# Optimization experiments

Measured on AMD Instinct MI355X. Metric: run time of the kernel, lower is better.

The kernel has to match this reference:

```python
import jax, jax.numpy as jnp
import numpy as np

N = 64        # SSM state size
L = 262144    # l_max / sequence length


def setup_inputs() -> dict:
    key = jax.random.key(0)
    ks = jax.random.split(key, 8)
    u = jax.random.normal(ks[0], (L,), dtype=jnp.float32)
    # HiPPO-DPLR style eigenvalue init
    Lambda_re = -0.5 * jnp.ones((N,), jnp.float32)
    Lambda_im = jnp.pi * jnp.arange(N, dtype=jnp.float32)
    P_re = jax.random.normal(ks[1], (N,), jnp.float32)
    P_im = jax.random.normal(ks[2], (N,), jnp.float32)
    B_re = jax.random.normal(ks[3], (N,), jnp.float32)
    B_im = jax.random.normal(ks[4], (N,), jnp.float32)
    C_ri = (0.5 ** 0.5) * jax.random.normal(ks[5], (N, 2), jnp.float32)  # C = C_ri[:,0] + i*C_ri[:,1]
    D = jnp.ones((1,), jnp.float32)
    log_step = jax.random.uniform(ks[6], (1,), jnp.float32,
                                  minval=float(np.log(0.001)), maxval=float(np.log(0.1)))
    return {"u": u, "Lambda_re": Lambda_re, "Lambda_im": Lambda_im,
            "P_re": P_re, "P_im": P_im, "B_re": B_re, "B_im": B_im,
            "C_ri": C_ri, "D": D, "log_step": log_step}


def _kernel_DPLR(Lambda, P, Q, B, C, step, l):
    # Evaluate the SSM generating function at the l roots of unity (bilinear discretization)
    Omega = jnp.exp((-2j * jnp.pi) * (jnp.arange(l) / l))          # (L,)
    g = (2.0 / step) * ((1.0 - Omega) / (1.0 + Omega))             # (L,)
    c = 2.0 / (1.0 + Omega)                                        # (L,)
    # Core Cauchy matrix: the single large (L, N) complex intermediate
    recip = 1.0 / (g[:, None] - Lambda[None, :])                   # (L, N)
    # Four Cauchy dot products fused into one thin matmul
    v = jnp.stack([C.conj() * B, C.conj() * P,
                   Q.conj() * B, Q.conj() * P], axis=1)            # (N, 4)
    k = recip @ v                                                  # (L, 4)
    k00, k01, k10, k11 = k[:, 0], k[:, 1], k[:, 2], k[:, 3]
    atRoots = c * (k00 - k01 * (1.0 / (1.0 + k11)) * k10)          # (L,)
    return jnp.fft.ifft(atRoots, l).real                           # (L,) real kernel


def _causal_convolution(u, K):
    l = u.shape[0]
    ud = jnp.fft.rfft(jnp.pad(u, (0, K.shape[0])))
    Kd = jnp.fft.rfft(jnp.pad(K, (0, l)))
    return jnp.fft.irfft(ud * Kd)[:l]


def reference(u, Lambda_re, Lambda_im, P_re, P_im, B_re, B_im, C_ri, D, log_step):
    Lambda = Lambda_re + 1j * Lambda_im
    P = P_re + 1j * P_im
    B = B_re + 1j * B_im
    C = C_ri[:, 0] + 1j * C_ri[:, 1]
    step = jnp.exp(log_step)                                       # (1,)
    K = _kernel_DPLR(Lambda, P, P, B, C, step, u.shape[0])
    return _causal_convolution(u, K) + D * u
```

## Files before the change

### kernel.cpp

```cpp
#include <hip/hip_runtime.h>
#include <math.h>

#define L_LEN  262144
#define NST    64
#define TPB    256
#define PI2F   6.2831853071795864769f
#define PIF    3.1415926535897932385f

__device__ inline float2 cmul(float2 a, float2 b) {
    return make_float2(a.x*b.x - a.y*b.y, a.x*b.y + a.y*b.x);
}

template<int M, int NF>
__device__ float2* lds_fft_r4(float2* b0, float2* b1, float sgn) {
    float2* src = b0; float2* dst = b1;
    int Ns = 1;
    while (Ns * 4 <= M) {
        __syncthreads();
        const int NB = NF * (M / 4);
        for (int bi = threadIdx.x; bi < NB; bi += TPB) {
            int f = bi / (M / 4);
            int j = bi & (M / 4 - 1);
            int r = j & (Ns - 1);
            const float2* s = src + f * M;
            float2 x0 = s[j];
            float2 x1 = s[j +     (M/4)];
            float2 x2 = s[j + 2 * (M/4)];
            float2 x3 = s[j + 3 * (M/4)];
            float ang = sgn * PI2F * ((float)r / (float)(4 * Ns));
            float sn, cs; __sincosf(ang, &sn, &cs);
            float2 w1 = make_float2(cs, sn);
            float2 w2 = cmul(w1, w1);
            float2 w3 = cmul(w2, w1);
            x1 = cmul(x1, w1); x2 = cmul(x2, w2); x3 = cmul(x3, w3);
            float2 t0 = make_float2(x0.x + x2.x, x0.y + x2.y);
            float2 t1 = make_float2(x0.x - x2.x, x0.y - x2.y);
            float2 t2 = make_float2(x1.x + x3.x, x1.y + x3.y);
            float2 t3 = make_float2(x1.x - x3.x, x1.y - x3.y);
            float2* d = dst + f * M + ((j - r) << 2) + r;
            d[0]      = make_float2(t0.x + t2.x, t0.y + t2.y);
            d[Ns]     = make_float2(t1.x - sgn * t3.y, t1.y + sgn * t3.x);
            d[2 * Ns] = make_float2(t0.x - t2.x, t0.y - t2.y);
            d[3 * Ns] = make_float2(t1.x + sgn * t3.y, t1.y - sgn * t3.x);
        }
        float2* t = src; src = dst; dst = t;
        Ns <<= 2;
    }
    if (Ns < M) {
        __syncthreads();
        const int NB = NF * (M / 2);
        for (int bi = threadIdx.x; bi < NB; bi += TPB) {
            int f = bi / (M / 2);
            int j = bi & (M / 2 - 1);
            const float2* s = src + f * M;
            float2 a = s[j];
            float2 b = s[j + M / 2];
            float ang = sgn * PI2F * ((float)j / (float)M);
            float sn, cs; __sincosf(ang, &sn, &cs);
            float2 wb = make_float2(cs * b.x - sn * b.y, cs * b.y + sn * b.x);
            float2* d = dst + f * M + j;
            d[0]     = make_float2(a.x + wb.x, a.y + wb.y);
            d[M / 2] = make_float2(a.x - wb.x, a.y - wb.y);
        }
        float2* t = src; src = dst; dst = t;
    }
    __syncthreads();
    return src;
}


__global__ __launch_bounds__(TPB) void k1_atroots(
    const float* __restrict__ Lre, const float* __restrict__ Lim,
    const float* __restrict__ Pre, const float* __restrict__ Pim,
    const float* __restrict__ Bre, const float* __restrict__ Bim,
    const float* __restrict__ Cri, const float* __restrict__ lstp,
    float2* __restrict__ Acm)
{
    __shared__ float4 cA[NST], cB[NST], cC[NST], cD[NST];
    const int t = threadIdx.x, bx = blockIdx.x;
    if (t < NST) {
        float lr = Lre[t], li = Lim[t];
        float pr = Pre[t], pi = Pim[t];
        float br = Bre[t], bi = Bim[t];
        float cr = Cri[2*t], ci = Cri[2*t+1];
        float dx = -lr;
        float v00x = cr*br + ci*bi, v00y = cr*bi - ci*br;
        float v01x = cr*pr + ci*pi, v01y = cr*pi - ci*pr;
        float v10x = pr*br + pi*bi, v10y = pr*bi - pi*br;
        float v11x = pr*pr + pi*pi;
        cA[t] = make_float4(li, dx*dx, dx*v11x, -v11x);
        cB[t] = make_float4(dx*v00x, v00y, dx*v00y, -v00x);
        cC[t] = make_float4(dx*v01x, v01y, dx*v01y, -v01x);
        cD[t] = make_float4(dx*v10x, v10y, dx*v10y, -v10x);
    }
    __syncthreads();
    const int c = bx >> 1;
    const int e = ((bx & 1) << 8) + t;
    const int j = c + (e << 9);
    const float invL = 1.0f / (float)L_LEN;
    float G2 = 2.0f / expf(lstp[0]);
    float h = PIF * ((float)j * invL);
    float sn, cs; __sincosf(h, &sn, &cs);
    float tn = sn * __frcp_rn(cs);
    tn = fminf(fmaxf(tn, -1e7f), 1e7f);
    float gi = G2 * tn;
    float k00x=0.f,k00y=0.f,k01x=0.f,k01y=0.f,k10x=0.f,k10y=0.f,k11x=0.f,k11y=0.f;
    #pragma unroll 4
    for (int n = 0; n < NST; ++n) {
        float4 a = cA[n];
        float dy   = gi - a.x;
        float iv   = __frcp_rn(fmaf(dy, dy, a.y));
        float ivdy = iv * dy;
        k11x = fmaf(iv, a.z, k11x);  k11y = fmaf(ivdy, a.w, k11y);
        float4 b = cB[n];
        k00x = fmaf(iv, b.x, fmaf(ivdy, b.y, k00x));
        k00y = fmaf(iv, b.z, fmaf(ivdy, b.w, k00y));
        float4 cc = cC[n];
        k01x = fmaf(iv, cc.x, fmaf(ivdy, cc.y, k01x));
        k01y = fmaf(iv, cc.z, fmaf(ivdy, cc.w, k01y));
        float4 d = cD[n];
        k10x = fmaf(iv, d.x, fmaf(ivdy, d.y, k10x));
        k10y = fmaf(iv, d.z, fmaf(ivdy, d.w, k10y));
    }
    float ax = 1.f + k11x, ay = k11y;
    float im = 1.f / (ax*ax + ay*ay);
    float tx = k01x*k10x - k01y*k10y;
    float ty = k01x*k10y + k01y*k10x;
    float wx = k00x - (tx*ax + ty*ay) * im;
    float wy = k00y - (ty*ax - tx*ay) * im;
    Acm[(c << 9) + e] = make_float2(wx - tn*wy, wy + tn*wx);
}

__global__ __launch_bounds__(TPB) void k2_pass1(
    const float* __restrict__ u, const float2* __restrict__ Acm,
    float2* __restrict__ T_K, float2* __restrict__ T_U, float2* __restrict__ T_Uo)
{
    __shared__ float2 b0[2048], b1[2048];
    const int t = threadIdx.x, bx = blockIdx.x;
    const int c0 = (bx & 255) << 1;
    const float invL = 1.0f / (float)L_LEN;
    if (bx < 256) {
        for (int i = t; i < 1024; i += TPB)
            b0[i] = Acm[((c0 + (i >> 9)) << 9) + (i & 511)];
        float2* r = lds_fft_r4<512, 2>(b0, b1, +1.f);
        for (int i = t; i < 1024; i += TPB) {
            int f = i & 1, k = i >> 1;
            int c = c0 + f;
            float ang = PI2F * ((float)(c * k) * invL);
            float sn, cs; __sincosf(ang, &sn, &cs);
            T_K[(k << 9) + c] = cmul(make_float2(cs, sn), r[(f << 9) + k]);
        }
    } else {
        for (int i = t; i < 1024; i += TPB) {
            int f = i & 1, e = i >> 1;
            int n = (c0 + f) + (e << 9);
            float uv = u[n];
            float sn, cs; __sincosf(PIF * ((float)n * invL), &sn, &cs);
            b0[(f << 9) + e]        = make_float2(uv, 0.f);
            b0[((2 + f) << 9) + e]  = make_float2(uv * cs, -uv * sn);
        }
        float2* r = lds_fft_r4<512, 4>(b0, b1, -1.f);
        for (int i = t; i < 2048; i += TPB) {
            int f = i & 1, k = (i >> 1) & 511, v = i >> 10;
            int c = c0 + f;
            float ang = -PI2F * ((float)(c * k) * invL);
            float sn, cs; __sincosf(ang, &sn, &cs);
            float2 val = cmul(make_float2(cs, sn), r[(((v << 1) + f) << 9) + k]);
            if (v == 0) T_U [(k << 9) + c] = val;
            else        T_Uo[(k << 9) + c] = val;
        }
    }
}

__global__ __launch_bounds__(TPB) void k3_mid(
    const float2* __restrict__ T_K, const float2* __restrict__ T_U,
    const float2* __restrict__ T_Uo,
    float2* __restrict__ T_Ko, float2* __restrict__ Ue, float2* __restrict__ Uo)
{
    __shared__ float2 b0[2048], b1[2048];
    const int t = threadIdx.x, bx = blockIdx.x;
    const int c0 = (bx & 255) << 1;
    const float invL = 1.0f / (float)L_LEN;
    if (bx < 256) {
        for (int i = t; i < 1024; i += TPB)
            b0[i] = T_K[((c0 + (i >> 9)) << 9) + (i & 511)];
        float2* r = lds_fft_r4<512, 2>(b0, b1, +1.f);
        float2* o = (r == b0) ? b1 : b0;
        for (int i = t; i < 1024; i += TPB) {
            int f = i >> 9, o1 = i & 511;
            int n = (c0 + f) + (o1 << 9);
            float K = r[i].x * invL;
            float sn, cs; __sincosf(PIF * ((float)n * invL), &sn, &cs);
            o[i] = make_float2(K * cs, -K * sn);
        }
        float2* r2 = lds_fft_r4<512, 2>(o, r, -1.f);
        for (int i = t; i < 1024; i += TPB) {
            int f = i & 1, k = i >> 1;
            int c = c0 + f;
            float ang = -PI2F * ((float)(c * k) * invL);
            float sn, cs; __sincosf(ang, &sn, &cs);
            T_Ko[(k << 9) + c] = cmul(make_float2(cs, sn), r2[(f << 9) + k]);
        }
    } else {
        for (int i = t; i < 2048; i += TPB) {
            int v = i >> 10, f = (i >> 9) & 1, e = i & 511;
            const float2* Tin = v ? T_Uo : T_U;
            b0[i] = Tin[((c0 + f) << 9) + e];
        }
        float2* r = lds_fft_r4<512, 4>(b0, b1, -1.f);
        for (int i = t; i < 2048; i += TPB) {
            int v = i >> 10, f = (i >> 9) & 1, k2 = i & 511;
            float2* Xo = v ? Uo : Ue;
            Xo[((c0 + f) << 9) + k2] = r[i];
        }
    }
}

__global__ __launch_bounds__(TPB) void k4_point_inv1(
    const float2* __restrict__ T_Ko, const float2* __restrict__ Ue,
    const float2* __restrict__ Uo, const float2* __restrict__ Acm,
    float2* __restrict__ T_Ve, float2* __restrict__ T_Vo)
{
    __shared__ float2 b0[2048], b1[2048];
    const int t = threadIdx.x, bx = blockIdx.x;
    const int kk0 = bx << 1;
    const float invL = 1.0f / (float)L_LEN;
    for (int i = t; i < 1024; i += TPB)
        b0[i] = T_Ko[((kk0 + (i >> 9)) << 9) + (i & 511)];
    float2* r = lds_fft_r4<512, 2>(b0, b1, -1.f);
    float2* o = (r == b0) ? b1 : b0;
    for (int i = t; i < 1024; i += TPB) {
        int f = i >> 9, k2 = i & 511;
        int kc = kk0 + f;
        float2 ko = r[i];
        float2 ue = Ue [(kc << 9) + k2];
        float2 uo = Uo [(kc << 9) + k2];
        float2 av = Acm[(kc << 9) + k2];
        o[i]        = cmul(ue, av);
        o[i + 1024] = cmul(uo, ko);
    }
    float2* r2 = lds_fft_r4<512, 4>(o, r, +1.f);
    for (int i = t; i < 2048; i += TPB) {
        int f = i & 1, k = (i >> 1) & 511, v = i >> 10;
        int c = kk0 + f;
        float ang = PI2F * ((float)(c * k) * invL);
        float sn, cs; __sincosf(ang, &sn, &cs);
        float2 val = cmul(make_float2(cs, sn), r2[(((v << 1) + f) << 9) + k]);
        if (v == 0) T_Ve[(k << 9) + c] = val;
        else        T_Vo[(k << 9) + c] = val;
    }
}

__global__ __launch_bounds__(TPB) void k5_out(
    const float2* __restrict__ T_Ve, const float2* __restrict__ T_Vo,
    const float* __restrict__ u, const float* __restrict__ Dp,
    float* __restrict__ out)
{
    __shared__ float2 b0[2048], b1[2048];
    const int t = threadIdx.x, bx = blockIdx.x;
    const int c0 = bx << 1;
    const float invL = 1.0f / (float)L_LEN;
    for (int i = t; i < 1024; i += TPB) {
        int f = i >> 9, m1 = i & 511;
        b0[i]        = T_Ve[((c0 + f) << 9) + m1];
        b0[i + 1024] = T_Vo[((c0 + f) << 9) + m1];
    }
    float2* r = lds_fft_r4<512, 4>(b0, b1, +1.f);
    const float sc = 0.5f * invL;
    const float D = Dp[0];
    for (int i = t; i < 1024; i += TPB) {
        int f = i & 1, o1 = i >> 1;
        int n = (c0 + f) + (o1 << 9);
        float sn, cs; __sincosf(PIF * ((float)n * invL), &sn, &cs);
        float2 yE = r[(f << 9) + o1];
        float2 yO = r[((f + 2) << 9) + o1];
        out[n] = fmaf(D, u[n], (yE.x + cs * yO.x - sn * yO.y) * sc);
    }
}

extern "C" void kernel_launch(void* const* d_in, const int* in_sizes, int n_in,
                              void* d_out, int out_size, void* d_ws, size_t ws_size,
                              hipStream_t stream) {
    const float* u    = (const float*)d_in[0];
    const float* Lre  = (const float*)d_in[1];
    const float* Lim  = (const float*)d_in[2];
    const float* Pre  = (const float*)d_in[3];
    const float* Pim  = (const float*)d_in[4];
    const float* Bre  = (const float*)d_in[5];
    const float* Bim  = (const float*)d_in[6];
    const float* Cri  = (const float*)d_in[7];
    const float* Dp   = (const float*)d_in[8];
    const float* lstp = (const float*)d_in[9];
    float* out = (float*)d_out;

    char* ws = (char*)d_ws;
    float2* Acm  = (float2*)(ws);
    float2* T_K  = (float2*)(ws + ( 2u << 20));
    float2* T_U  = (float2*)(ws + ( 4u << 20));
    float2* T_Uo = (float2*)(ws + ( 6u << 20));
    float2* T_Ko = (float2*)(ws + ( 8u << 20));
    float2* Ue   = (float2*)(ws + (10u << 20));
    float2* Uo   = (float2*)(ws + (12u << 20));
    float2* T_Ve = (float2*)(ws + (14u << 20));
    float2* T_Vo = (float2*)(ws + (16u << 20));

    k1_atroots <<<1024, TPB, 0, stream>>>(Lre,Lim,Pre,Pim,Bre,Bim,Cri,lstp, Acm);
    k2_pass1   <<< 512, TPB, 0, stream>>>(u, Acm, T_K, T_U, T_Uo);
    k3_mid     <<< 512, TPB, 0, stream>>>(T_K, T_U, T_Uo, T_Ko, Ue, Uo);
    k4_point_inv1<<<256, TPB, 0, stream>>>(T_Ko, Ue, Uo, Acm, T_Ve, T_Vo);
    k5_out     <<< 256, TPB, 0, stream>>>(T_Ve, T_Vo, u, Dp, out);
}
```

Before: 124.0 us.

## Fuse Cauchy atRoots evaluation into first FFT pass and halve per-block work downstream

The Cauchy-kernel evaluation kernel is merged into the first FFT pass. Each block computes its 1024 generating-function values in registers, four points per thread, and writes them straight into LDS as well as to global memory, which removes one kernel launch and the Acm reload. The last two kernels now process one column per block instead of two, doubling the grid to 512 blocks so more CUs are busy. The risks are higher register pressure from the 4x8 accumulators and the extra compute in the fused blocks, which may unbalance them against the u-FFT blocks.

```diff
diff --git a/kernel.cpp b/kernel.cpp
--- a/kernel.cpp
+++ b/kernel.cpp
@@ -69,79 +69,84 @@
 }
 
 
-__global__ __launch_bounds__(TPB) void k1_atroots(
+__global__ __launch_bounds__(TPB) void kI(
+    const float* __restrict__ u,
     const float* __restrict__ Lre, const float* __restrict__ Lim,
     const float* __restrict__ Pre, const float* __restrict__ Pim,
     const float* __restrict__ Bre, const float* __restrict__ Bim,
     const float* __restrict__ Cri, const float* __restrict__ lstp,
-    float2* __restrict__ Acm)
-{
-    __shared__ float4 cA[NST], cB[NST], cC[NST], cD[NST];
-    const int t = threadIdx.x, bx = blockIdx.x;
-    if (t < NST) {
-        float lr = Lre[t], li = Lim[t];
-        float pr = Pre[t], pi = Pim[t];
-        float br = Bre[t], bi = Bim[t];
-        float cr = Cri[2*t], ci = Cri[2*t+1];
-        float dx = -lr;
-        float v00x = cr*br + ci*bi, v00y = cr*bi - ci*br;
-        float v01x = cr*pr + ci*pi, v01y = cr*pi - ci*pr;
-        float v10x = pr*br + pi*bi, v10y = pr*bi - pi*br;
-        float v11x = pr*pr + pi*pi;
-        cA[t] = make_float4(li, dx*dx, dx*v11x, -v11x);
-        cB[t] = make_float4(dx*v00x, v00y, dx*v00y, -v00x);
-        cC[t] = make_float4(dx*v01x, v01y, dx*v01y, -v01x);
-        cD[t] = make_float4(dx*v10x, v10y, dx*v10y, -v10x);
-    }
-    __syncthreads();
-    const int c = bx >> 1;
-    const int e = ((bx & 1) << 8) + t;
-    const int j = c + (e << 9);
-    const float invL = 1.0f / (float)L_LEN;
-    float G2 = 2.0f / expf(lstp[0]);
-    float h = PIF * ((float)j * invL);
-    float sn, cs; __sincosf(h, &sn, &cs);
-    float tn = sn * __frcp_rn(cs);
-    tn = fminf(fmaxf(tn, -1e7f), 1e7f);
-    float gi = G2 * tn;
-    float k00x=0.f,k00y=0.f,k01x=0.f,k01y=0.f,k10x=0.f,k10y=0.f,k11x=0.f,k11y=0.f;
-    #pragma unroll 4
-    for (int n = 0; n < NST; ++n) {
-        float4 a = cA[n];
-        float dy   = gi - a.x;
-        float iv   = __frcp_rn(fmaf(dy, dy, a.y));
-        float ivdy = iv * dy;
-        k11x = fmaf(iv, a.z, k11x);  k11y = fmaf(ivdy, a.w, k11y);
-        float4 b = cB[n];
-        k00x = fmaf(iv, b.x, fmaf(ivdy, b.y, k00x));
-        k00y = fmaf(iv, b.z, fmaf(ivdy, b.w, k00y));
-        float4 cc = cC[n];
-        k01x = fmaf(iv, cc.x, fmaf(ivdy, cc.y, k01x));
-        k01y = fmaf(iv, cc.z, fmaf(ivdy, cc.w, k01y));
-        float4 d = cD[n];
-        k10x = fmaf(iv, d.x, fmaf(ivdy, d.y, k10x));
-        k10y = fmaf(iv, d.z, fmaf(ivdy, d.w, k10y));
-    }
-    float ax = 1.f + k11x, ay = k11y;
-    float im = 1.f / (ax*ax + ay*ay);
-    float tx = k01x*k10x - k01y*k10y;
-    float ty = k01x*k10y + k01y*k10x;
-    float wx = k00x - (tx*ax + ty*ay) * im;
-    float wy = k00y - (ty*ax - tx*ay) * im;
-    Acm[(c << 9) + e] = make_float2(wx - tn*wy, wy + tn*wx);
-}
-
-__global__ __launch_bounds__(TPB) void k2_pass1(
-    const float* __restrict__ u, const float2* __restrict__ Acm,
-    float2* __restrict__ T_K, float2* __restrict__ T_U, float2* __restrict__ T_Uo)
+    float2* __restrict__ Acm, float2* __restrict__ T_K,
+    float2* __restrict__ T_U, float2* __restrict__ T_Uo)
 {
     __shared__ float2 b0[2048], b1[2048];
+    __shared__ float4 cA[NST], cB[NST], cC[NST], cD[NST];
     const int t = threadIdx.x, bx = blockIdx.x;
     const int c0 = (bx & 255) << 1;
     const float invL = 1.0f / (float)L_LEN;
     if (bx < 256) {
-        for (int i = t; i < 1024; i += TPB)
-            b0[i] = Acm[((c0 + (i >> 9)) << 9) + (i & 511)];
+        if (t < NST) {
+            float lr = Lre[t], li = Lim[t];
+            float pr = Pre[t], pi = Pim[t];
+            float br = Bre[t], bi = Bim[t];
+            float cr = Cri[2*t], ci = Cri[2*t+1];
+            float dx = -lr;
+            float v00x = cr*br + ci*bi, v00y = cr*bi - ci*br;
+            float v01x = cr*pr + ci*pi, v01y = cr*pi - ci*pr;
+            float v10x = pr*br + pi*bi, v10y = pr*bi - pi*br;
+            float v11x = pr*pr + pi*pi;
+            cA[t] = make_float4(li, dx*dx, dx*v11x, -v11x);
+            cB[t] = make_float4(dx*v00x, v00y, dx*v00y, -v00x);
+            cC[t] = make_float4(dx*v01x, v01y, dx*v01y, -v01x);
+            cD[t] = make_float4(dx*v10x, v10y, dx*v10y, -v10x);
+        }
+        __syncthreads();
+        float G2 = 2.0f / expf(lstp[0]);
+        float tn[4], gi[4], acc[4][8];
+        #pragma unroll
+        for (int p = 0; p < 4; ++p) {
+            int i = t + (p << 8);
+            int f = i >> 9, e = i & 511;
+            int m = (c0 + f) + (e << 9);
+            float h = PIF * ((float)m * invL);
+            float sn, cs; __sincosf(h, &sn, &cs);
+            float tv = sn * __frcp_rn(cs);
+            tv = fminf(fmaxf(tv, -1e7f), 1e7f);
+            tn[p] = tv; gi[p] = G2 * tv;
+            #pragma unroll
+            for (int q = 0; q < 8; ++q) acc[p][q] = 0.f;
+        }
+        #pragma unroll 2
+        for (int n = 0; n < NST; ++n) {
+            float4 a = cA[n], b = cB[n], cc = cC[n], d = cD[n];
+            #pragma unroll
+            for (int p = 0; p < 4; ++p) {
+                float dy   = gi[p] - a.x;
+                float iv   = __frcp_rn(fmaf(dy, dy, a.y));
+                float ivdy = iv * dy;
+                acc[p][6] = fmaf(iv, a.z, acc[p][6]);
+                acc[p][7] = fmaf(ivdy, a.w, acc[p][7]);
+                acc[p][0] = fmaf(iv, b.x,  fmaf(ivdy, b.y,  acc[p][0]));
+                acc[p][1] = fmaf(iv, b.z,  fmaf(ivdy, b.w,  acc[p][1]));
+                acc[p][2] = fmaf(iv, cc.x, fmaf(ivdy, cc.y, acc[p][2]));
+                acc[p][3] = fmaf(iv, cc.z, fmaf(ivdy, cc.w, acc[p][3]));
+                acc[p][4] = fmaf(iv, d.x,  fmaf(ivdy, d.y,  acc[p][4]));
+                acc[p][5] = fmaf(iv, d.z,  fmaf(ivdy, d.w,  acc[p][5]));
+            }
+        }
+        #pragma unroll
+        for (int p = 0; p < 4; ++p) {
+            int i = t + (p << 8);
+            int f = i >> 9, e = i & 511;
+            float ax = 1.f + acc[p][6], ay = acc[p][7];
+            float im = 1.f / (ax*ax + ay*ay);
+            float tx = acc[p][2]*acc[p][4] - acc[p][3]*acc[p][5];
+            float ty = acc[p][2]*acc[p][5] + acc[p][3]*acc[p][4];
+            float wx = acc[p][0] - (tx*ax + ty*ay) * im;
+            float wy = acc[p][1] - (ty*ax - tx*ay) * im;
+            float2 A = make_float2(wx - tn[p]*wy, wy + tn[p]*wx);
+            Acm[((c0 + f) << 9) + e] = A;
+            b0[i] = A;
+        }
         float2* r = lds_fft_r4<512, 2>(b0, b1, +1.f);
         for (int i = t; i < 1024; i += TPB) {
             int f = i & 1, k = i >> 1;
@@ -156,8 +161,8 @@
             int n = (c0 + f) + (e << 9);
             float uv = u[n];
             float sn, cs; __sincosf(PIF * ((float)n * invL), &sn, &cs);
-            b0[(f << 9) + e]        = make_float2(uv, 0.f);
-            b0[((2 + f) << 9) + e]  = make_float2(uv * cs, -uv * sn);
+            b0[(f << 9) + e]       = make_float2(uv, 0.f);
+            b0[((2 + f) << 9) + e] = make_float2(uv * cs, -uv * sn);
         }
         float2* r = lds_fft_r4<512, 4>(b0, b1, -1.f);
         for (int i = t; i < 2048; i += TPB) {
@@ -172,7 +177,7 @@
     }
 }
 
-__global__ __launch_bounds__(TPB) void k3_mid(
+__global__ __launch_bounds__(TPB) void kII(
     const float2* __restrict__ T_K, const float2* __restrict__ T_U,
     const float2* __restrict__ T_Uo,
     float2* __restrict__ T_Ko, float2* __restrict__ Ue, float2* __restrict__ Uo)
@@ -216,64 +221,57 @@
     }
 }
 
-__global__ __launch_bounds__(TPB) void k4_point_inv1(
+__global__ __launch_bounds__(TPB) void kIII(
     const float2* __restrict__ T_Ko, const float2* __restrict__ Ue,
     const float2* __restrict__ Uo, const float2* __restrict__ Acm,
     float2* __restrict__ T_Ve, float2* __restrict__ T_Vo)
 {
-    __shared__ float2 b0[2048], b1[2048];
-    const int t = threadIdx.x, bx = blockIdx.x;
-    const int kk0 = bx << 1;
+    __shared__ float2 b0[1024], b1[1024];
+    const int t = threadIdx.x, kc = blockIdx.x;
     const float invL = 1.0f / (float)L_LEN;
-    for (int i = t; i < 1024; i += TPB)
-        b0[i] = T_Ko[((kk0 + (i >> 9)) << 9) + (i & 511)];
-    float2* r = lds_fft_r4<512, 2>(b0, b1, -1.f);
+    for (int i = t; i < 512; i += TPB)
+        b0[i] = T_Ko[(kc << 9) + i];
+    float2* r = lds_fft_r4<512, 1>(b0, b1, -1.f);
     float2* o = (r == b0) ? b1 : b0;
+    for (int i = t; i < 512; i += TPB) {
+        float2 ko = r[i];
+        float2 ue = Ue [(kc << 9) + i];
+        float2 uo = Uo [(kc << 9) + i];
+        float2 av = Acm[(kc << 9) + i];
+        o[i]       = cmul(ue, av);
+        o[i + 512] = cmul(uo, ko);
+    }
+    float2* r2 = lds_fft_r4<512, 2>(o, r, +1.f);
     for (int i = t; i < 1024; i += TPB) {
-        int f = i >> 9, k2 = i & 511;
-        int kc = kk0 + f;
-        float2 ko = r[i];
-        float2 ue = Ue [(kc << 9) + k2];
-        float2 uo = Uo [(kc << 9) + k2];
-        float2 av = Acm[(kc << 9) + k2];
-        o[i]        = cmul(ue, av);
-        o[i + 1024] = cmul(uo, ko);
-    }
-    float2* r2 = lds_fft_r4<512, 4>(o, r, +1.f);
-    for (int i = t; i < 2048; i += TPB) {
-        int f = i & 1, k = (i >> 1) & 511, v = i >> 10;
-        int c = kk0 + f;
-        float ang = PI2F * ((float)(c * k) * invL);
+        int v = i >> 9, k = i & 511;
+        float ang = PI2F * ((float)(kc * k) * invL);
         float sn, cs; __sincosf(ang, &sn, &cs);
-        float2 val = cmul(make_float2(cs, sn), r2[(((v << 1) + f) << 9) + k]);
-        if (v == 0) T_Ve[(k << 9) + c] = val;
-        else        T_Vo[(k << 9) + c] = val;
-    }
-}
-
-__global__ __launch_bounds__(TPB) void k5_out(
+        float2 val = cmul(make_float2(cs, sn), r2[(v << 9) + k]);
+        if (v == 0) T_Ve[(k << 9) + kc] = val;
+        else        T_Vo[(k << 9) + kc] = val;
+    }
+}
+
+__global__ __launch_bounds__(TPB) void kIV(
     const float2* __restrict__ T_Ve, const float2* __restrict__ T_Vo,
     const float* __restrict__ u, const float* __restrict__ Dp,
     float* __restrict__ out)
 {
-    __shared__ float2 b0[2048], b1[2048];
-    const int t = threadIdx.x, bx = blockIdx.x;
-    const int c0 = bx << 1;
+    __shared__ float2 b0[1024], b1[1024];
+    const int t = threadIdx.x, k = blockIdx.x;
     const float invL = 1.0f / (float)L_LEN;
-    for (int i = t; i < 1024; i += TPB) {
-        int f = i >> 9, m1 = i & 511;
-        b0[i]        = T_Ve[((c0 + f) << 9) + m1];
-        b0[i + 1024] = T_Vo[((c0 + f) << 9) + m1];
-    }
-    float2* r = lds_fft_r4<512, 4>(b0, b1, +1.f);
+    for (int i = t; i < 512; i += TPB) {
+        b0[i]       = T_Ve[(k << 9) + i];
+        b0[i + 512] = T_Vo[(k << 9) + i];
+    }
+    float2* r = lds_fft_r4<512, 2>(b0, b1, +1.f);
     const float sc = 0.5f * invL;
     const float D = Dp[0];
-    for (int i = t; i < 1024; i += TPB) {
-        int f = i & 1, o1 = i >> 1;
-        int n = (c0 + f) + (o1 << 9);
+    for (int o1 = t; o1 < 512; o1 += TPB) {
+        int n = k + (o1 << 9);
         float sn, cs; __sincosf(PIF * ((float)n * invL), &sn, &cs);
-        float2 yE = r[(f << 9) + o1];
-        float2 yO = r[((f + 2) << 9) + o1];
+        float2 yE = r[o1];
+        float2 yO = r[o1 + 512];
         out[n] = fmaf(D, u[n], (yE.x + cs * yO.x - sn * yO.y) * sc);
     }
 }
@@ -304,9 +302,9 @@
     float2* T_Ve = (float2*)(ws + (14u << 20));
     float2* T_Vo = (float2*)(ws + (16u << 20));
 
-    k1_atroots <<<1024, TPB, 0, stream>>>(Lre,Lim,Pre,Pim,Bre,Bim,Cri,lstp, Acm);
-    k2_pass1   <<< 512, TPB, 0, stream>>>(u, Acm, T_K, T_U, T_Uo);
-    k3_mid     <<< 512, TPB, 0, stream>>>(T_K, T_U, T_Uo, T_Ko, Ue, Uo);
-    k4_point_inv1<<<256, TPB, 0, stream>>>(T_Ko, Ue, Uo, Acm, T_Ve, T_Vo);
-    k5_out     <<< 256, TPB, 0, stream>>>(T_Ve, T_Vo, u, Dp, out);
-}
+    kI  <<<512, TPB, 0, stream>>>(u, Lre,Lim,Pre,Pim,Bre,Bim,Cri,lstp,
+                                  Acm, T_K, T_U, T_Uo);
+    kII <<<512, TPB, 0, stream>>>(T_K, T_U, T_Uo, T_Ko, Ue, Uo);
+    kIII<<<512, TPB, 0, stream>>>(T_Ko, Ue, Uo, Acm, T_Ve, T_Vo);
+    kIV <<<512, TPB, 0, stream>>>(T_Ve, T_Vo, u, Dp, out);
+}
```

Measured after the change: 117.7 us. -5.1%, faster.
